# Optimization experiments

Hardware: AMD Instinct MI355X
Metric: run time of the kernel (lower is better)

Reference implementation:

```python
import jax, jax.numpy as jnp
import numpy as np

N_NODES = 50000
N_EDGES = 600000
N_GRAPHS = 64
D_IN = 128
D_HID = 128
D_LAT = 64
BN_EPS = 1e-5


def setup_inputs() -> dict:
    key = jax.random.key(0)
    ks = jax.random.split(key, 8)
    x = jax.random.normal(ks[0], (N_NODES, D_IN), dtype=jnp.float32)
    edge_index = jax.random.randint(ks[1], (2, N_EDGES), 0, N_NODES, dtype=jnp.int64 if jax.config.jax_enable_x64 else jnp.int32)
    batch = jnp.sort(jax.random.randint(ks[2], (N_NODES,), 0, N_GRAPHS))
    d_cat = 13 * D_IN  # x + (mean,max,min,std) x (identity,amp,att)
    s = 1.0 / np.sqrt(d_cat)
    W0 = jax.random.normal(ks[3], (d_cat, D_HID), dtype=jnp.float32) * s
    W1 = jax.random.normal(ks[4], (13 * D_HID, D_HID), dtype=jnp.float32) * s
    W2 = jax.random.normal(ks[5], (13 * D_HID, D_HID), dtype=jnp.float32) * s
    fcW = jax.random.normal(ks[6], (D_HID, D_LAT), dtype=jnp.float32) * (1.0 / np.sqrt(D_HID))
    return {
        "x": x, "edge_index": edge_index, "batch": batch,
        "W0": W0, "b0": jnp.zeros((D_HID,), jnp.float32),
        "W1": W1, "b1": jnp.zeros((D_HID,), jnp.float32),
        "W2": W2, "b2": jnp.zeros((D_HID,), jnp.float32),
        "bn_gamma": jnp.ones((D_HID,), jnp.float32),
        "bn_beta": jnp.zeros((D_HID,), jnp.float32),
        "fcW": fcW, "fcb": jnp.zeros((D_LAT,), jnp.float32),
    }


def _pna_conv(h, W, b, src, dst, deg, delta):
    # h: [N, d]; messages gathered from source nodes per edge: [E, d]
    m = h[src]
    cnt = jnp.maximum(deg, 1.0)[:, None]
    ssum = jax.ops.segment_sum(m, dst, num_segments=N_NODES)
    mean = ssum / cnt
    ssq = jax.ops.segment_sum(m * m, dst, num_segments=N_NODES)
    std = jnp.sqrt(jnp.maximum(ssq / cnt - mean * mean, 0.0) + 1e-5)
    mx = jax.ops.segment_max(m, dst, num_segments=N_NODES)
    mn = jax.ops.segment_min(m, dst, num_segments=N_NODES)
    has = (deg > 0)[:, None]
    mx = jnp.where(has, mx, 0.0)
    mn = jnp.where(has, mn, 0.0)
    agg = jnp.concatenate([mean, mx, mn, std], axis=-1)  # [N, 4d]
    logd = jnp.log(deg + 1.0)[:, None]
    amp = logd / delta
    att = delta / jnp.maximum(logd, 1e-5)
    feat = jnp.concatenate([h, agg, agg * amp, agg * att], axis=-1)  # [N, 13d]
    return feat @ W + b


def reference(x, edge_index, batch, W0, b0, W1, b1, W2, b2, bn_gamma, bn_beta, fcW, fcb):
    src, dst = edge_index[0], edge_index[1]
    deg = jax.ops.segment_sum(jnp.ones((src.shape[0],), x.dtype), dst, num_segments=N_NODES)
    delta = jnp.mean(jnp.log(deg + 1.0))  # avg log-degree normalizer
    h = jax.nn.relu(_pna_conv(x, W0, b0, src, dst, deg, delta))
    h = jax.nn.relu(_pna_conv(h, W1, b1, src, dst, deg, delta))
    h = jax.nn.relu(_pna_conv(h, W2, b2, src, dst, deg, delta))
    # dropout is identity in eval mode
    pooled = jax.ops.segment_sum(h, batch, num_segments=N_GRAPHS)  # global_add_pool
    mu = jnp.mean(pooled, axis=0)
    var = jnp.var(pooled, axis=0)
    bn = (pooled - mu) / jnp.sqrt(var + BN_EPS) * bn_gamma + bn_beta
    return bn @ fcW + fcb
```

## Files before the change

### kernel.cpp

```cpp
#include <hip/hip_runtime.h>
#include <cstdint>
#include <cstddef>

#define N_NODESC 50000
#define N_PAD    50048
#define N_EDGESC 600000
#define N_GRAPHSC 64
#define D_HIDC   128
#define D_LATC   64
#define D_G      640
#define D_WROW   1664

typedef unsigned short u16;
typedef unsigned int   u32;

typedef _Float16 f16x8 __attribute__((ext_vector_type(8)));
typedef _Float16 f16x2 __attribute__((ext_vector_type(2)));
typedef float    f32x4 __attribute__((ext_vector_type(4)));
typedef float    f32x2 __attribute__((ext_vector_type(2)));

__device__ __forceinline__ u16 f2h(float f) {
    return __builtin_bit_cast(u16, (_Float16)f);
}
__device__ __forceinline__ float h2f(u16 u) {
    return (float)__builtin_bit_cast(_Float16, u);
}

__device__ __forceinline__ void gll16(void* lds, const void* g) {
    __builtin_amdgcn_global_load_lds(
        (const __attribute__((address_space(1))) void*)g,
        (__attribute__((address_space(3))) void*)lds, 16, 0, 0);
}

__global__ void __launch_bounds__(256) k_setup(
        const float* __restrict__ x, const float* __restrict__ W0,
        const float* __restrict__ W1, const float* __restrict__ W2,
        const int* __restrict__ batch,
        u16* __restrict__ h, u16* __restrict__ Wt,
        int* __restrict__ zero_base, int nz, int ZB, int* __restrict__ goff) {
    int b = blockIdx.x;
    int t = threadIdx.x;
    if (b < ZB) {
        int i = b * 256 + t;
        if (i < nz) zero_base[i] = 0;
        return;
    }
    b -= ZB;
    if (b < 12500) {
        int i = b * 256 + t;
        float2 v = ((const float2*)x)[i];
        ((u32*)h)[i] = (u32)f2h(v.x) | ((u32)f2h(v.y) << 16);
        return;
    }
    b -= 12500;
    if (b < 2496) {
        int which = b / 832;
        int i = (b % 832) * 256 + t;
        const float* W = (which == 0) ? W0 : (which == 1) ? W1 : W2;
        int k = i / D_HIDC, j = i % D_HIDC;
        Wt[(size_t)which * D_WROW * D_HIDC + (size_t)j * D_WROW + k] = f2h(W[i]);
        return;
    }
    int g = t;
    if (g <= N_GRAPHSC) {
        int lo = 0, hi = N_NODESC;
        while (lo < hi) {
            int mid = (lo + hi) >> 1;
            if (batch[mid] < g) lo = mid + 1; else hi = mid;
        }
        goff[g] = lo;
    }
}

__global__ void k_count(const int* __restrict__ dst, int* __restrict__ deg) {
    int e = blockIdx.x * 256 + threadIdx.x;
    if (e < N_EDGESC) atomicAdd(&deg[dst[e]], 1);
}

__global__ void __launch_bounds__(256) k_scan_part(
        const int* __restrict__ deg, int* __restrict__ bsum,
        float* __restrict__ lsum) {
    __shared__ int s[256];
    __shared__ float ls[256];
    int idx = blockIdx.x * 256 + threadIdx.x;
    int v = (idx < N_NODESC) ? deg[idx] : 0;
    s[threadIdx.x] = v;
    ls[threadIdx.x] = (idx < N_NODESC) ? logf((float)v + 1.0f) : 0.0f;
    __syncthreads();
    for (int o = 128; o > 0; o >>= 1) {
        if (threadIdx.x < o) {
            s[threadIdx.x] += s[threadIdx.x + o];
            ls[threadIdx.x] += ls[threadIdx.x + o];
        }
        __syncthreads();
    }
    if (threadIdx.x == 0) { bsum[blockIdx.x] = s[0]; lsum[blockIdx.x] = ls[0]; }
}

__global__ void __launch_bounds__(256) k_scan_block(
        int* __restrict__ bsum, const float* __restrict__ lsum,
        float* __restrict__ delta_p) {
    __shared__ int s[256];
    __shared__ float ls[256];
    int t = threadIdx.x;
    int v = (t < 196) ? bsum[t] : 0;
    s[t] = v;
    ls[t] = (t < 196) ? lsum[t] : 0.0f;
    __syncthreads();
    for (int o = 1; o < 256; o <<= 1) {
        int add = (t >= o) ? s[t - o] : 0;
        __syncthreads();
        s[t] += add;
        __syncthreads();
    }
    if (t < 196) bsum[t] = s[t] - v;
    for (int o = 128; o > 0; o >>= 1) {
        if (t < o) ls[t] += ls[t + o];
        __syncthreads();
    }
    if (t == 0) delta_p[0] = ls[0] * (1.0f / (float)N_NODESC);
}

__global__ void __launch_bounds__(256) k_scan_final(
        const int* __restrict__ deg, const int* __restrict__ bsum,
        int* __restrict__ row_off) {
    __shared__ int s[256];
    int t = threadIdx.x;
    int idx = blockIdx.x * 256 + t;
    int v = (idx < N_NODESC) ? deg[idx] : 0;
    s[t] = v; __syncthreads();
    for (int o = 1; o < 256; o <<= 1) {
        int add = (t >= o) ? s[t - o] : 0;
        __syncthreads();
        s[t] += add;
        __syncthreads();
    }
    int excl = s[t] - v + bsum[blockIdx.x];
    if (idx < N_NODESC) row_off[idx] = excl;
    if (idx == 0) row_off[N_NODESC] = N_EDGESC;
}

__global__ void k_fill_csr(const int* __restrict__ src, const int* __restrict__ dst,
                           const int* __restrict__ row_off, int* __restrict__ cursor,
                           int* __restrict__ csr_src) {
    int e = blockIdx.x * 256 + threadIdx.x;
    if (e < N_EDGESC) {
        int d = dst[e];
        int pos = row_off[d] + atomicAdd(&cursor[d], 1);
        csr_src[pos] = src[e];
    }
}


__global__ void __launch_bounds__(256) k_aggregate(
        const u16* __restrict__ h, const int* __restrict__ row_off,
        const int* __restrict__ csr_src, u16* __restrict__ G) {
    int n = blockIdx.x * 4 + (threadIdx.x >> 6);
    if (n >= N_NODESC) return;
    int lane = threadIdx.x & 63;
    int half = lane >> 5, l32 = lane & 31;
    int c4 = 4 * l32;
    int beg = row_off[n], end = row_off[n + 1];
    const _Float16 NEG = (_Float16)(-65504.0f), POS = (_Float16)(65504.0f);
    f32x2 s01 = {0.f, 0.f}, s23 = {0.f, 0.f};
    f32x2 q01 = {0.f, 0.f}, q23 = {0.f, 0.f};
    f16x2 mx01 = {NEG, NEG}, mx23 = {NEG, NEG};
    f16x2 mn01 = {POS, POS}, mn23 = {POS, POS};

    #define PROC(u) { \
        f16x2 p01 = __builtin_bit_cast(f16x2, (u).x); \
        f16x2 p23 = __builtin_bit_cast(f16x2, (u).y); \
        f32x2 c01 = __builtin_convertvector(p01, f32x2); \
        f32x2 c23 = __builtin_convertvector(p23, f32x2); \
        s01 += c01; s23 += c23; \
        q01 += c01 * c01; q23 += c23 * c23; \
        mx01 = __builtin_elementwise_max(mx01, p01); \
        mx23 = __builtin_elementwise_max(mx23, p23); \
        mn01 = __builtin_elementwise_min(mn01, p01); \
        mn23 = __builtin_elementwise_min(mn23, p23); }

    int i = beg + half;
    for (; i + 6 < end; i += 8) {
        int e0 = csr_src[i],     e1 = csr_src[i + 2];
        int e2 = csr_src[i + 4], e3 = csr_src[i + 6];
        uint2 u0 = *(const uint2*)(h + (size_t)e0 * D_HIDC + c4);
        uint2 u1 = *(const uint2*)(h + (size_t)e1 * D_HIDC + c4);
        uint2 u2 = *(const uint2*)(h + (size_t)e2 * D_HIDC + c4);
        uint2 u3 = *(const uint2*)(h + (size_t)e3 * D_HIDC + c4);
        PROC(u0); PROC(u1); PROC(u2); PROC(u3);
    }
    for (; i < end; i += 2) {
        int e0 = csr_src[i];
        uint2 u0 = *(const uint2*)(h + (size_t)e0 * D_HIDC + c4);
        PROC(u0);
    }
    #undef PROC

    s01.x += __shfl_xor(s01.x, 32); s01.y += __shfl_xor(s01.y, 32);
    s23.x += __shfl_xor(s23.x, 32); s23.y += __shfl_xor(s23.y, 32);
    q01.x += __shfl_xor(q01.x, 32); q01.y += __shfl_xor(q01.y, 32);
    q23.x += __shfl_xor(q23.x, 32); q23.y += __shfl_xor(q23.y, 32);
    #define MRG(v, OP) v = OP(v, \
        __builtin_bit_cast(f16x2, __shfl_xor(__builtin_bit_cast(int, v), 32)))
    MRG(mx01, __builtin_elementwise_max); MRG(mx23, __builtin_elementwise_max);
    MRG(mn01, __builtin_elementwise_min); MRG(mn23, __builtin_elementwise_min);
    #undef MRG

    int d = end - beg;
    float inv = 1.0f / fmaxf((float)d, 1.0f);
    float me0 = s01.x * inv, me1 = s01.y * inv;
    float me2 = s23.x * inv, me3 = s23.y * inv;
    float sd0 = sqrtf(fmaxf(q01.x * inv - me0 * me0, 0.0f) + 1e-5f);
    float sd1 = sqrtf(fmaxf(q01.y * inv - me1 * me1, 0.0f) + 1e-5f);
    float sd2 = sqrtf(fmaxf(q23.x * inv - me2 * me2, 0.0f) + 1e-5f);
    float sd3 = sqrtf(fmaxf(q23.y * inv - me3 * me3, 0.0f) + 1e-5f);
    float fx0 = (float)mx01.x, fx1 = (float)mx01.y;
    float fx2 = (float)mx23.x, fx3 = (float)mx23.y;
    float fn0 = (float)mn01.x, fn1 = (float)mn01.y;
    float fn2 = (float)mn23.x, fn3 = (float)mn23.y;
    if (d == 0) {
        fx0 = fx1 = fx2 = fx3 = 0.0f;
        fn0 = fn1 = fn2 = fn3 = 0.0f;
    }
    u16* base = G + (size_t)n * D_G;
    #define PK2(a, b) ((u32)f2h(a) | ((u32)f2h(b) << 16))
    if (half == 0) {
        *(uint2*)(base + c4) = *(const uint2*)(h + (size_t)n * D_HIDC + c4);
        uint2 m; m.x = PK2(me0, me1); m.y = PK2(me2, me3);
        *(uint2*)(base + 128 + c4) = m;
        uint2 X; X.x = PK2(fx0, fx1); X.y = PK2(fx2, fx3);
        *(uint2*)(base + 256 + c4) = X;
    } else {
        uint2 N_; N_.x = PK2(fn0, fn1); N_.y = PK2(fn2, fn3);
        *(uint2*)(base + 384 + c4) = N_;
        uint2 S; S.x = PK2(sd0, sd1); S.y = PK2(sd2, sd3);
        *(uint2*)(base + 512 + c4) = S;
    }
    #undef PK2
}

__global__ void __launch_bounds__(256, 2) k_gemm(
        const u16* __restrict__ G, const u16* __restrict__ Wt,
        const int* __restrict__ deg, const float* __restrict__ delta_p,
        const float* __restrict__ bias, u16* __restrict__ hout) {
    __shared__ _Float16 A1[128 * 64];
    __shared__ _Float16 A2[128 * 64];
    __shared__ _Float16 A3[128 * 64];
    __shared__ _Float16 Bt[128 * 64];
    const _Float16* Wf = (const _Float16*)Wt;
    const _Float16* Gf = (const _Float16*)G;
    int n0 = blockIdx.x * 128;
    int t = threadIdx.x;
    int w = t >> 6, lane = t & 63;
    int srow8 = lane >> 3, sslot = lane & 7;
    int stg = (sslot ^ srow8) * 8;
    int q4 = lane >> 4, r16 = lane & 15;
    int sx0 = (q4 ^ (lane & 7)) * 8;
    int sx1 = ((q4 + 4) ^ (lane & 7)) * 8;
    int col = lane & 15;

    float delta = delta_p[0];
    float atv[8];
    _Float16 amh[8];
    #pragma unroll
    for (int nt = 0; nt < 8; nt++) {
        int node = n0 + nt * 16 + col;
        float logd = logf((float)deg[node] + 1.0f);
        amh[nt] = (_Float16)(logd / delta);
        atv[nt] = delta / fmaxf(logd, 1e-5f);
    }

    f32x4 acc[2][8], ac3[2][8];
    #pragma unroll
    for (int a = 0; a < 2; a++)
        #pragma unroll
        for (int b = 0; b < 8; b++) {
            acc[a][b] = (f32x4){0.f, 0.f, 0.f, 0.f};
            ac3[a][b] = (f32x4){0.f, 0.f, 0.f, 0.f};
        }

    for (int ki = 0; ki < 10; ki++) {
        int k0 = ki * 64;
        bool sreg = (k0 >= 128);
        __syncthreads();
        #pragma unroll
        for (int r = 0; r < 4; r++) {
            int rr = r * 4 + w;
            const _Float16* wrow = Wf + (size_t)(rr * 8 + srow8) * D_WROW;
            gll16(&A1[rr * 512], wrow + k0 + stg);
        }
        if (sreg) {
            #pragma unroll
            for (int r = 0; r < 4; r++) {
                int rr = r * 4 + w;
                const _Float16* wrow = Wf + (size_t)(rr * 8 + srow8) * D_WROW;
                gll16(&A2[rr * 512], wrow + 512 + k0 + stg);
                gll16(&A3[rr * 512], wrow + 1024 + k0 + stg);
            }
        }
        #pragma unroll
        for (int q = 0; q < 4; q++) {
            int rr = q * 4 + w;
            gll16(&Bt[rr * 512], Gf + (size_t)(n0 + rr * 8 + srow8) * D_G + k0 + stg);
        }
        __syncthreads();
        f16x8 a00 = *(const f16x8*)&A1[(w * 32 + r16) * 64 + sx0];
        f16x8 a01 = *(const f16x8*)&A1[(w * 32 + r16) * 64 + sx1];
        f16x8 a10 = *(const f16x8*)&A1[(w * 32 + 16 + r16) * 64 + sx0];
        f16x8 a11 = *(const f16x8*)&A1[(w * 32 + 16 + r16) * 64 + sx1];
        if (!sreg) {
            #pragma unroll
            for (int nt = 0; nt < 8; nt++) {
                f16x8 b0 = *(const f16x8*)&Bt[(nt * 16 + r16) * 64 + sx0];
                f16x8 b1 = *(const f16x8*)&Bt[(nt * 16 + r16) * 64 + sx1];
                acc[0][nt] = __builtin_amdgcn_mfma_f32_16x16x32_f16(a00, b0, acc[0][nt], 0, 0, 0);
                acc[1][nt] = __builtin_amdgcn_mfma_f32_16x16x32_f16(a10, b0, acc[1][nt], 0, 0, 0);
                acc[0][nt] = __builtin_amdgcn_mfma_f32_16x16x32_f16(a01, b1, acc[0][nt], 0, 0, 0);
                acc[1][nt] = __builtin_amdgcn_mfma_f32_16x16x32_f16(a11, b1, acc[1][nt], 0, 0, 0);
            }
        } else {
            f16x8 w2a0 = *(const f16x8*)&A2[(w * 32 + r16) * 64 + sx0];
            f16x8 w2a1 = *(const f16x8*)&A2[(w * 32 + r16) * 64 + sx1];
            f16x8 w2b0 = *(const f16x8*)&A2[(w * 32 + 16 + r16) * 64 + sx0];
            f16x8 w2b1 = *(const f16x8*)&A2[(w * 32 + 16 + r16) * 64 + sx1];
            f16x8 w3a0 = *(const f16x8*)&A3[(w * 32 + r16) * 64 + sx0];
            f16x8 w3a1 = *(const f16x8*)&A3[(w * 32 + r16) * 64 + sx1];
            f16x8 w3b0 = *(const f16x8*)&A3[(w * 32 + 16 + r16) * 64 + sx0];
            f16x8 w3b1 = *(const f16x8*)&A3[(w * 32 + 16 + r16) * 64 + sx1];
            #pragma unroll
            for (int nt = 0; nt < 8; nt++) {
                f16x8 b0 = *(const f16x8*)&Bt[(nt * 16 + r16) * 64 + sx0];
                f16x8 b1 = *(const f16x8*)&Bt[(nt * 16 + r16) * 64 + sx1];
                f16x8 bm0 = b0 * amh[nt];
                f16x8 bm1 = b1 * amh[nt];
                acc[0][nt] = __builtin_amdgcn_mfma_f32_16x16x32_f16(a00, b0, acc[0][nt], 0, 0, 0);
                acc[1][nt] = __builtin_amdgcn_mfma_f32_16x16x32_f16(a10, b0, acc[1][nt], 0, 0, 0);
                acc[0][nt] = __builtin_amdgcn_mfma_f32_16x16x32_f16(a01, b1, acc[0][nt], 0, 0, 0);
                acc[1][nt] = __builtin_amdgcn_mfma_f32_16x16x32_f16(a11, b1, acc[1][nt], 0, 0, 0);
                acc[0][nt] = __builtin_amdgcn_mfma_f32_16x16x32_f16(w2a0, bm0, acc[0][nt], 0, 0, 0);
                acc[1][nt] = __builtin_amdgcn_mfma_f32_16x16x32_f16(w2b0, bm0, acc[1][nt], 0, 0, 0);
                acc[0][nt] = __builtin_amdgcn_mfma_f32_16x16x32_f16(w2a1, bm1, acc[0][nt], 0, 0, 0);
                acc[1][nt] = __builtin_amdgcn_mfma_f32_16x16x32_f16(w2b1, bm1, acc[1][nt], 0, 0, 0);
                ac3[0][nt] = __builtin_amdgcn_mfma_f32_16x16x32_f16(w3a0, b0, ac3[0][nt], 0, 0, 0);
                ac3[1][nt] = __builtin_amdgcn_mfma_f32_16x16x32_f16(w3b0, b0, ac3[1][nt], 0, 0, 0);
                ac3[0][nt] = __builtin_amdgcn_mfma_f32_16x16x32_f16(w3a1, b1, ac3[0][nt], 0, 0, 0);
                ac3[1][nt] = __builtin_amdgcn_mfma_f32_16x16x32_f16(w3b1, b1, ac3[1][nt], 0, 0, 0);
            }
        }
    }
    int rowq = q4 * 4;
    #pragma unroll
    for (int nt = 0; nt < 8; nt++) {
        int node = n0 + nt * 16 + col;
        float at = atv[nt];
        #pragma unroll
        for (int mt = 0; mt < 2; mt++) {
            int jb = w * 32 + mt * 16 + rowq;
            f32x4 v = acc[mt][nt], v3 = ac3[mt][nt];
            ushort4 o;
            o.x = f2h(fmaxf(v.x + at * v3.x + bias[jb], 0.0f));
            o.y = f2h(fmaxf(v.y + at * v3.y + bias[jb + 1], 0.0f));
            o.z = f2h(fmaxf(v.z + at * v3.z + bias[jb + 2], 0.0f));
            o.w = f2h(fmaxf(v.w + at * v3.w + bias[jb + 3], 0.0f));
            *(ushort4*)&hout[(size_t)node * D_HIDC + jb] = o;
        }
    }
}


__global__ void __launch_bounds__(256) k_pool(
        const u16* __restrict__ h, const int* __restrict__ goff,
        float* __restrict__ pooled) {
    __shared__ float sm[256];
    int g = blockIdx.x >> 2, s = blockIdx.x & 3;
    int gb = goff[g], ge = goff[g + 1];
    int len = ge - gb;
    int q = (len + 3) >> 2;
    int nb = gb + s * q;
    int ne = min(nb + q, ge);
    int t = threadIdx.x;
    int j = t & 127, half = t >> 7;
    float acc = 0.0f;
    for (int n = nb + half; n < ne; n += 2)
        acc += h2f(h[(size_t)n * D_HIDC + j]);
    sm[t] = acc; __syncthreads();
    if (t < 128) {
        float v = sm[t] + sm[t + 128];
        atomicAdd(&pooled[g * D_HIDC + j], v);
    }
}

__global__ void __launch_bounds__(128) k_bn_fc(
        const float* __restrict__ pooled, const float* __restrict__ gamma,
        const float* __restrict__ beta, const float* __restrict__ fcW,
        const float* __restrict__ fcb, float* __restrict__ out) {
    __shared__ float bn[D_HIDC];
    int g = blockIdx.x, t = threadIdx.x;
    float s = 0.f, q = 0.f;
    for (int gg = 0; gg < N_GRAPHSC; gg++) {
        float v = pooled[gg * D_HIDC + t];
        s += v; q += v * v;
    }
    float mu = s * (1.0f / N_GRAPHSC);
    float var = q * (1.0f / N_GRAPHSC) - mu * mu;
    float inv = 1.0f / sqrtf(var + 1e-5f);
    bn[t] = (pooled[g * D_HIDC + t] - mu) * inv * gamma[t] + beta[t];
    __syncthreads();
    if (t < D_LATC) {
        float accum = fcb[t];
        for (int j = 0; j < D_HIDC; j++) accum += bn[j] * fcW[j * D_LATC + t];
        out[g * D_LATC + t] = accum;
    }
}


extern "C" void kernel_launch(void* const* d_in, const int* in_sizes, int n_in,
                              void* d_out, int out_size, void* d_ws, size_t ws_size,
                              hipStream_t stream) {
    const float* x     = (const float*)d_in[0];
    const int*   ei    = (const int*)d_in[1];
    const int*   batch = (const int*)d_in[2];
    const float* W0 = (const float*)d_in[3];
    const float* b0 = (const float*)d_in[4];
    const float* W1 = (const float*)d_in[5];
    const float* b1 = (const float*)d_in[6];
    const float* W2 = (const float*)d_in[7];
    const float* b2 = (const float*)d_in[8];
    const float* gamma = (const float*)d_in[9];
    const float* beta  = (const float*)d_in[10];
    const float* fcW   = (const float*)d_in[11];
    const float* fcb   = (const float*)d_in[12];
    float* out = (float*)d_out;
    const int* srcv = ei;
    const int* dstv = ei + N_EDGESC;

    char* p = (char*)d_ws;
    auto alloc = [&](size_t bytes) -> char* {
        char* r = p;
        p += (bytes + 255) & ~(size_t)255;
        return r;
    };
    int*   deg_cnt = (int*)alloc((size_t)N_PAD * 4);
    int*   cursor  = (int*)alloc((size_t)N_NODESC * 4);
    float* delta_p = (float*)alloc(4);
    float* pooled  = (float*)alloc((size_t)N_GRAPHSC * D_HIDC * 4);
    char*  zero_end = p;
    int*   row_off = (int*)alloc((size_t)(N_NODESC + 1) * 4);
    int*   goff    = (int*)alloc((size_t)(N_GRAPHSC + 1) * 4);
    int*   bsum    = (int*)alloc(256 * 4);
    float* lsum    = (float*)alloc(256 * 4);
    int*   csr_src = (int*)alloc((size_t)N_EDGESC * 4);
    u16*   Wt      = (u16*)alloc((size_t)3 * D_WROW * D_HIDC * 2);
    u16*   hA      = (u16*)alloc((size_t)N_PAD * D_HIDC * 2);
    u16*   hB      = (u16*)alloc((size_t)N_PAD * D_HIDC * 2);
    u16*   G       = (u16*)alloc((size_t)N_PAD * D_G * 2);

    int nz = (int)((zero_end - (char*)deg_cnt) / 4);
    int ZB = (nz + 255) / 256;
    int setup_grid = ZB + 12500 + 2496 + 1;
    k_setup<<<setup_grid, 256, 0, stream>>>(x, W0, W1, W2, batch,
                                            hB, Wt, deg_cnt, nz, ZB, goff);
    k_count<<<(N_EDGESC + 255) / 256, 256, 0, stream>>>(dstv, deg_cnt);
    k_scan_part<<<196, 256, 0, stream>>>(deg_cnt, bsum, lsum);
    k_scan_block<<<1, 256, 0, stream>>>(bsum, lsum, delta_p);
    k_scan_final<<<196, 256, 0, stream>>>(deg_cnt, bsum, row_off);
    k_fill_csr<<<(N_EDGESC + 255) / 256, 256, 0, stream>>>(srcv, dstv, row_off, cursor, csr_src);

    const float* bs[3] = {b0, b1, b2};
    const u16* h_in[3]  = {hB, hA, hB};
    u16*       h_out[3] = {hA, hB, hA};
    size_t wsz = (size_t)D_WROW * D_HIDC;
    for (int l = 0; l < 3; l++) {
        k_aggregate<<<(N_NODESC + 3) / 4, 256, 0, stream>>>(
            h_in[l], row_off, csr_src, G);
        k_gemm<<<N_PAD / 128, 256, 0, stream>>>(
            G, Wt + (size_t)l * wsz, deg_cnt, delta_p, bs[l], h_out[l]);
    }
    k_pool<<<4 * N_GRAPHSC, 256, 0, stream>>>(h_out[2], goff, pooled);
    k_bn_fc<<<N_GRAPHSC, 128, 0, stream>>>(pooled, gamma, beta, fcW, fcb, out);
}
```

Before: 405.0 us.

## Drop self-feature copy from G buffer, prescale CSR indices, use packed f32 ops

```diff
diff --git a/kernel.cpp b/kernel.cpp
--- a/kernel.cpp
+++ b/kernel.cpp
@@ -8,7 +8,7 @@
 #define N_GRAPHSC 64
 #define D_HIDC   128
 #define D_LATC   64
-#define D_G      640
+#define D_GS     512
 #define D_WROW   1664
 
 typedef unsigned short u16;
@@ -24,6 +24,17 @@
 }
 __device__ __forceinline__ float h2f(u16 u) {
     return (float)__builtin_bit_cast(_Float16, u);
+}
+
+__device__ __forceinline__ f32x2 pk_add(f32x2 a, f32x2 b) {
+    f32x2 d;
+    asm("v_pk_add_f32 %0, %1, %2" : "=v"(d) : "v"(a), "v"(b));
+    return d;
+}
+__device__ __forceinline__ f32x2 pk_fma(f32x2 a, f32x2 b, f32x2 c) {
+    f32x2 d;
+    asm("v_pk_fma_f32 %0, %1, %2, %3" : "=v"(d) : "v"(a), "v"(b), "v"(c));
+    return d;
 }
 
 __device__ __forceinline__ void gll16(void* lds, const void* g) {
@@ -147,7 +158,7 @@
     if (e < N_EDGESC) {
         int d = dst[e];
         int pos = row_off[d] + atomicAdd(&cursor[d], 1);
-        csr_src[pos] = src[e];
+        csr_src[pos] = src[e] << 8;
     }
 }
 
@@ -160,6 +171,8 @@
     int lane = threadIdx.x & 63;
     int half = lane >> 5, l32 = lane & 31;
     int c4 = 4 * l32;
+    u32 c8 = 8u * (u32)l32;
+    const char* h8 = (const char*)h;
     int beg = row_off[n], end = row_off[n + 1];
     const _Float16 NEG = (_Float16)(-65504.0f), POS = (_Float16)(65504.0f);
     f32x2 s01 = {0.f, 0.f}, s23 = {0.f, 0.f};
@@ -172,8 +185,8 @@
         f16x2 p23 = __builtin_bit_cast(f16x2, (u).y); \
         f32x2 c01 = __builtin_convertvector(p01, f32x2); \
         f32x2 c23 = __builtin_convertvector(p23, f32x2); \
-        s01 += c01; s23 += c23; \
-        q01 += c01 * c01; q23 += c23 * c23; \
+        s01 = pk_add(s01, c01); s23 = pk_add(s23, c23); \
+        q01 = pk_fma(c01, c01, q01); q23 = pk_fma(c23, c23, q23); \
         mx01 = __builtin_elementwise_max(mx01, p01); \
         mx23 = __builtin_elementwise_max(mx23, p23); \
         mn01 = __builtin_elementwise_min(mn01, p01); \
@@ -181,17 +194,17 @@
 
     int i = beg + half;
     for (; i + 6 < end; i += 8) {
-        int e0 = csr_src[i],     e1 = csr_src[i + 2];
-        int e2 = csr_src[i + 4], e3 = csr_src[i + 6];
-        uint2 u0 = *(const uint2*)(h + (size_t)e0 * D_HIDC + c4);
-        uint2 u1 = *(const uint2*)(h + (size_t)e1 * D_HIDC + c4);
-        uint2 u2 = *(const uint2*)(h + (size_t)e2 * D_HIDC + c4);
-        uint2 u3 = *(const uint2*)(h + (size_t)e3 * D_HIDC + c4);
+        u32 e0 = (u32)csr_src[i],     e1 = (u32)csr_src[i + 2];
+        u32 e2 = (u32)csr_src[i + 4], e3 = (u32)csr_src[i + 6];
+        uint2 u0 = *(const uint2*)(h8 + (e0 + c8));
+        uint2 u1 = *(const uint2*)(h8 + (e1 + c8));
+        uint2 u2 = *(const uint2*)(h8 + (e2 + c8));
+        uint2 u3 = *(const uint2*)(h8 + (e3 + c8));
         PROC(u0); PROC(u1); PROC(u2); PROC(u3);
     }
     for (; i < end; i += 2) {
-        int e0 = csr_src[i];
-        uint2 u0 = *(const uint2*)(h + (size_t)e0 * D_HIDC + c4);
+        u32 e0 = (u32)csr_src[i];
+        uint2 u0 = *(const uint2*)(h8 + (e0 + c8));
         PROC(u0);
     }
     #undef PROC
@@ -222,25 +235,25 @@
         fx0 = fx1 = fx2 = fx3 = 0.0f;
         fn0 = fn1 = fn2 = fn3 = 0.0f;
     }
-    u16* base = G + (size_t)n * D_G;
+    u16* base = G + (size_t)n * D_GS;
     #define PK2(a, b) ((u32)f2h(a) | ((u32)f2h(b) << 16))
     if (half == 0) {
-        *(uint2*)(base + c4) = *(const uint2*)(h + (size_t)n * D_HIDC + c4);
         uint2 m; m.x = PK2(me0, me1); m.y = PK2(me2, me3);
-        *(uint2*)(base + 128 + c4) = m;
+        *(uint2*)(base + c4) = m;
         uint2 X; X.x = PK2(fx0, fx1); X.y = PK2(fx2, fx3);
-        *(uint2*)(base + 256 + c4) = X;
+        *(uint2*)(base + 128 + c4) = X;
     } else {
         uint2 N_; N_.x = PK2(fn0, fn1); N_.y = PK2(fn2, fn3);
-        *(uint2*)(base + 384 + c4) = N_;
+        *(uint2*)(base + 256 + c4) = N_;
         uint2 S; S.x = PK2(sd0, sd1); S.y = PK2(sd2, sd3);
-        *(uint2*)(base + 512 + c4) = S;
+        *(uint2*)(base + 384 + c4) = S;
     }
     #undef PK2
 }
 
 __global__ void __launch_bounds__(256, 2) k_gemm(
-        const u16* __restrict__ G, const u16* __restrict__ Wt,
+        const u16* __restrict__ hin, const u16* __restrict__ G,
+        const u16* __restrict__ Wt,
         const int* __restrict__ deg, const float* __restrict__ delta_p,
         const float* __restrict__ bias, u16* __restrict__ hout) {
     __shared__ _Float16 A1[128 * 64];
@@ -249,6 +262,7 @@
     __shared__ _Float16 Bt[128 * 64];
     const _Float16* Wf = (const _Float16*)Wt;
     const _Float16* Gf = (const _Float16*)G;
+    const _Float16* Hf = (const _Float16*)hin;
     int n0 = blockIdx.x * 128;
     int t = threadIdx.x;
     int w = t >> 6, lane = t & 63;
@@ -301,7 +315,11 @@
         #pragma unroll
         for (int q = 0; q < 4; q++) {
             int rr = q * 4 + w;
-            gll16(&Bt[rr * 512], Gf + (size_t)(n0 + rr * 8 + srow8) * D_G + k0 + stg);
+            int row = n0 + rr * 8 + srow8;
+            const _Float16* bsrc = (!sreg)
+                ? Hf + (size_t)row * D_HIDC + k0 + stg
+                : Gf + (size_t)row * D_GS + (k0 - 128) + stg;
+            gll16(&Bt[rr * 512], bsrc);
         }
         __syncthreads();
         f16x8 a00 = *(const f16x8*)&A1[(w * 32 + r16) * 64 + sx0];
@@ -453,7 +471,7 @@
     u16*   Wt      = (u16*)alloc((size_t)3 * D_WROW * D_HIDC * 2);
     u16*   hA      = (u16*)alloc((size_t)N_PAD * D_HIDC * 2);
     u16*   hB      = (u16*)alloc((size_t)N_PAD * D_HIDC * 2);
-    u16*   G       = (u16*)alloc((size_t)N_PAD * D_G * 2);
+    u16*   G       = (u16*)alloc((size_t)N_PAD * D_GS * 2);
 
     int nz = (int)((zero_end - (char*)deg_cnt) / 4);
     int ZB = (nz + 255) / 256;
@@ -474,7 +492,7 @@
         k_aggregate<<<(N_NODESC + 3) / 4, 256, 0, stream>>>(
             h_in[l], row_off, csr_src, G);
         k_gemm<<<N_PAD / 128, 256, 0, stream>>>(
-            G, Wt + (size_t)l * wsz, deg_cnt, delta_p, bs[l], h_out[l]);
+            h_in[l], G, Wt + (size_t)l * wsz, deg_cnt, delta_p, bs[l], h_out[l]);
     }
     k_pool<<<4 * N_GRAPHSC, 256, 0, stream>>>(h_out[2], goff, pooled);
     k_bn_fc<<<N_GRAPHSC, 128, 0, stream>>>(pooled, gamma, beta, fcW, fcb, out);
```

New measurement: 396.2 us. 2.2% less time.
